# Kernel tuning notes

Hardware: AMD Instinct MI355X
Metric: run time of the kernel (lower is better)

Reference implementation:

```python
import jax, jax.numpy as jnp
import numpy as np


def _pairwise_upper_dists(x):
    # x: [N, D] -> distances for all i<j pairs, shape [N*(N-1)/2]
    n = x.shape[0]
    sq = jnp.sum(x * x, axis=-1)                      # [N]
    d2 = sq[:, None] + sq[None, :] - 2.0 * (x @ x.T)  # [N, N]
    d2 = jnp.maximum(d2, 0.0)
    iu, ju = jnp.triu_indices(n, k=1)                 # matches combinations(range(n), 2)
    return jnp.sqrt(d2[iu, ju])


def setup_inputs() -> dict:
    key = jax.random.key(0)
    k1, k2 = jax.random.split(key)
    pred = jax.random.normal(k1, (1024, 8192), dtype=jnp.float32)
    target = jax.random.normal(k2, (1024, 8192), dtype=jnp.float32)
    return {"pred": pred, "target": target}


def reference(pred, target):
    # all_pairs_in_batch=True branch: Euclidean distance per pair, MSE between
    # the pred-distance vector and the target-distance vector.
    pred_d = _pairwise_upper_dists(pred)      # [P]
    target_d = _pairwise_upper_dists(target)  # [P]
    return jnp.mean((pred_d - target_d) ** 2)
```

## Files before the change

### kernel.cpp

```cpp
#include <hip/hip_runtime.h>
#include <hip/hip_bf16.h>
#include <hip/hip_fp16.h>

#define D 8192
#define NPAIR 523776.0

typedef short short8 __attribute__((ext_vector_type(8)));
typedef float f32x4 __attribute__((ext_vector_type(4)));
typedef _Float16 f16x8 __attribute__((ext_vector_type(8)));

__device__ __forceinline__ short8 cvt8(const float4 a, const float4 b) {
    union { short8 s; __hip_bfloat162 h[4]; } u;
    u.h[0] = __float22bfloat162_rn(make_float2(a.x, a.y));
    u.h[1] = __float22bfloat162_rn(make_float2(a.z, a.w));
    u.h[2] = __float22bfloat162_rn(make_float2(b.x, b.y));
    u.h[3] = __float22bfloat162_rn(make_float2(b.z, b.w));
    return u.s;
}

__device__ __forceinline__ void decode_bid(int bid, int& m, int& ti, int& tj, int& k0, int& nsteps) {
    int x = bid & 7, s = bid >> 3;
    m = x >> 2;
    int xr = x & 3;
    if (s < 16) {
        ti = tj = s & 7;
        int c = ((s >> 3) << 2) + xr;
        k0 = c * 1024; nsteps = 32;
    } else {
        int sp = s - 16;
        int c = (sp / 28) * 4 + xr;
        int tt = sp % 28;
        int a = 0;
        while (tt >= 7 - a) { tt -= 7 - a; ++a; }
        ti = a; tj = a + 1 + tt;
        k0 = c * 512; nsteps = 16;
    }
}
__device__ __forceinline__ int bid_off(int m, int tt, int c) {
    return (m * 4 + (c & 3)) + ((16 + (c >> 2) * 28 + tt) << 3);
}
__device__ __forceinline__ int bid_diag(int m, int dt, int c) {
    return (m * 4 + (c & 3)) + ((((c >> 2) << 3) + dt) << 3);
}

#define GRAM_STEP(S, RA, RB) { \
    const int cur_ = (S) & 1; \
    const short* __restrict__ bufA = lsA[cur_]; \
    const short* __restrict__ bufB = same ? lsA[cur_] : lsB[cur_]; \
    __builtin_amdgcn_s_setprio(1); \
    short8 bf0 = *(const short8*)((const char*)bufB + (rbB + kby)); \
    short8 bf1 = *(const short8*)((const char*)bufB + (rbB + 1024 + kby)); \
    _Pragma("unroll") \
    for (int mi = 0; mi < 4; ++mi) { \
        short8 af = *(const short8*)((const char*)bufA + (rbA + mi * 1024 + kby)); \
        acc[mi][0] = __builtin_amdgcn_mfma_f32_16x16x32_bf16(af, bf0, acc[mi][0], 0, 0, 0); \
        acc[mi][1] = __builtin_amdgcn_mfma_f32_16x16x32_bf16(af, bf1, acc[mi][1], 0, 0, 0); \
    } \
    __builtin_amdgcn_s_setprio(0); \
    if ((S) + 1 < nsteps) { \
        const int nxt_ = cur_ ^ 1; \
        *(short8*)((char*)lsA[nxt_] + wby) = cvt8(RA[0], RA[1]); \
        if (!same) *(short8*)((char*)lsB[nxt_] + wby) = cvt8(RB[0], RB[1]); \
        if ((S) + 3 < nsteps) { \
            const float4* p_ = (const float4*)(gA + ((S) + 3) * 32); \
            RA[0] = p_[0]; RA[1] = p_[1]; \
            if (!same) { \
                const float4* q_ = (const float4*)(gB + ((S) + 3) * 32); \
                RB[0] = q_[0]; RB[1] = q_[1]; \
            } \
        } \
    } \
    asm volatile("s_waitcnt lgkmcnt(0)" ::: "memory"); \
    __builtin_amdgcn_s_barrier(); \
}

template<bool STORE>
__global__ __launch_bounds__(512, 4)
void gram_kernel(const float* __restrict__ pred, const float* __restrict__ tgt,
                 void* __restrict__ outv, float* __restrict__ norms) {
    int m, ti, tj, k0, nsteps;
    decode_bid(blockIdx.x, m, ti, tj, k0, nsteps);
    const bool same = (ti == tj);
    const float* __restrict__ x = m ? tgt : pred;

    __shared__ short lsA[2][4096];
    __shared__ short lsB[2][4096];

    const int tid = threadIdx.x;
    const int lane = tid & 63;
    const int wid = tid >> 6;
    const int wr = wid >> 2, wc = wid & 3;

    const int srow = tid >> 2, sc8 = tid & 3;
    const float* __restrict__ gA = x + (size_t)(ti * 128 + srow) * D + k0 + sc8 * 8;
    const float* __restrict__ gB = x + (size_t)(tj * 128 + srow) * D + k0 + sc8 * 8;
    const int wby = srow * 64 + ((sc8 ^ ((srow >> 1) & 3)) << 4);

    const int rbA = (wr * 64 + (lane & 15)) * 64;
    const int rbB = (wc * 32 + (lane & 15)) * 64;
    const int kby = (((lane >> 4) ^ (((lane & 15) >> 1) & 3)) << 4);

    f32x4 zero = {0.f, 0.f, 0.f, 0.f};
    f32x4 acc[4][2];
#pragma unroll
    for (int mi = 0; mi < 4; ++mi) { acc[mi][0] = zero; acc[mi][1] = zero; }

    float4 raX[2], rbX[2], raY[2], rbY[2];

    { const float4* p = (const float4*)gA; raX[0] = p[0]; raX[1] = p[1];
      if (!same) { const float4* q = (const float4*)gB; rbX[0] = q[0]; rbX[1] = q[1]; } }
    *(short8*)((char*)lsA[0] + wby) = cvt8(raX[0], raX[1]);
    if (!same) *(short8*)((char*)lsB[0] + wby) = cvt8(rbX[0], rbX[1]);
    { const float4* p = (const float4*)(gA + 32); raX[0] = p[0]; raX[1] = p[1];
      if (!same) { const float4* q = (const float4*)(gB + 32); rbX[0] = q[0]; rbX[1] = q[1]; } }
    { const float4* p = (const float4*)(gA + 64); raY[0] = p[0]; raY[1] = p[1];
      if (!same) { const float4* q = (const float4*)(gB + 64); rbY[0] = q[0]; rbY[1] = q[1]; } }
    asm volatile("s_waitcnt lgkmcnt(0)" ::: "memory");
    __builtin_amdgcn_s_barrier();

    for (int sp = 0; sp < nsteps; sp += 2) {
        GRAM_STEP(sp,     raX, rbX)
        GRAM_STEP(sp + 1, raY, rbY)
    }

    if (STORE) {
        __half* __restrict__ dst = (__half*)outv + (size_t)blockIdx.x * 16384;
#pragma unroll
        for (int mi = 0; mi < 4; ++mi)
#pragma unroll
            for (int ni = 0; ni < 2; ++ni)
#pragma unroll
                for (int r = 0; r < 4; ++r) {
                    int li = wr * 64 + mi * 16 + (lane >> 4) * 4 + r;
                    int lj = wc * 32 + ni * 16 + (lane & 15);
                    dst[li * 128 + lj] = __float2half_rn(acc[mi][ni][r]);
                    if (same && li == lj)
                        atomicAdd(&norms[m * 1024 + ti * 128 + li], acc[mi][ni][r]);
                }
    } else {
        float* __restrict__ g = (float*)outv + (size_t)m * (1024 * 1024);
#pragma unroll
        for (int mi = 0; mi < 4; ++mi)
#pragma unroll
            for (int ni = 0; ni < 2; ++ni)
#pragma unroll
                for (int r = 0; r < 4; ++r) {
                    int gi = ti * 128 + wr * 64 + mi * 16 + (lane >> 4) * 4 + r;
                    int gj = tj * 128 + wc * 32 + ni * 16 + (lane & 15);
                    atomicAdd(&g[gi * 1024 + gj], acc[mi][ni][r]);
                }
    }
}

__global__ __launch_bounds__(256)
void loss_store_kernel(const __half* __restrict__ part, const float* __restrict__ norms,
                       float* __restrict__ partial) {
    const int tid = threadIdx.x;
    const int sid = blockIdx.x * 256 + tid;
    const int i  = sid >> 7;
    const int j0 = (sid & 127) << 3;
    float local = 0.f;
    if (j0 + 7 > i) {
        const int ti = i >> 7, tj = j0 >> 7;
        const int el = ((i & 127) << 7) + (j0 & 127);
        float gp[8] = {0,0,0,0,0,0,0,0}, gt[8] = {0,0,0,0,0,0,0,0};
        if (ti == tj) {
#pragma unroll
            for (int c = 0; c < 8; ++c) {
                f16x8 vp = *(const f16x8*)(part + (size_t)bid_diag(0, ti, c) * 16384 + el);
                f16x8 vt = *(const f16x8*)(part + (size_t)bid_diag(1, ti, c) * 16384 + el);
#pragma unroll
                for (int e = 0; e < 8; ++e) { gp[e] += (float)vp[e]; gt[e] += (float)vt[e]; }
            }
        } else {
            int tt = 7 * ti - (ti * (ti - 1)) / 2 + (tj - ti - 1);
#pragma unroll
            for (int c = 0; c < 16; ++c) {
                f16x8 vp = *(const f16x8*)(part + (size_t)bid_off(0, tt, c) * 16384 + el);
                f16x8 vt = *(const f16x8*)(part + (size_t)bid_off(1, tt, c) * 16384 + el);
#pragma unroll
                for (int e = 0; e < 8; ++e) { gp[e] += (float)vp[e]; gt[e] += (float)vt[e]; }
            }
        }
        const float nip = norms[i], nit = norms[1024 + i];
        const float4 njp0 = *(const float4*)(norms + j0);
        const float4 njp1 = *(const float4*)(norms + j0 + 4);
        const float4 njt0 = *(const float4*)(norms + 1024 + j0);
        const float4 njt1 = *(const float4*)(norms + 1024 + j0 + 4);
        const float njp[8] = {njp0.x, njp0.y, njp0.z, njp0.w, njp1.x, njp1.y, njp1.z, njp1.w};
        const float njt[8] = {njt0.x, njt0.y, njt0.z, njt0.w, njt1.x, njt1.y, njt1.z, njt1.w};
#pragma unroll
        for (int e = 0; e < 8; ++e) {
            int j = j0 + e;
            if (j > i) {
                float dp = nip + njp[e] - 2.f * gp[e];
                float dt = nit + njt[e] - 2.f * gt[e];
                float c2 = sqrtf(fmaxf(dp, 0.f)) - sqrtf(fmaxf(dt, 0.f));
                local += c2 * c2;
            }
        }
    }
#pragma unroll
    for (int off = 32; off > 0; off >>= 1) local += __shfl_down(local, off);
    __shared__ float wsum[4];
    if ((tid & 63) == 0) wsum[tid >> 6] = local;
    __syncthreads();
    if (tid == 0) partial[blockIdx.x] = wsum[0] + wsum[1] + wsum[2] + wsum[3];
}

__global__ __launch_bounds__(256)
void loss_atomic_kernel(const float* __restrict__ gram, float* __restrict__ partial) {
    const float* __restrict__ gP = gram;
    const float* __restrict__ gT = gram + 1024 * 1024;
    const int tid = threadIdx.x;
    const int base = blockIdx.x * 256 + tid;
    float local = 0.f;
#pragma unroll
    for (int s = 0; s < 4; ++s) {
        int lin = base + s * 262144;
        int i = lin >> 10, j = lin & 1023;
        if (j > i) {
            float dp = gP[i * 1024 + i] + gP[j * 1024 + j] - 2.f * gP[lin];
            float dt = gT[i * 1024 + i] + gT[j * 1024 + j] - 2.f * gT[lin];
            float c = sqrtf(fmaxf(dp, 0.f)) - sqrtf(fmaxf(dt, 0.f));
            local += c * c;
        }
    }
#pragma unroll
    for (int off = 32; off > 0; off >>= 1) local += __shfl_down(local, off);
    __shared__ float wsum[4];
    if ((tid & 63) == 0) wsum[tid >> 6] = local;
    __syncthreads();
    if (tid == 0) partial[blockIdx.x] = wsum[0] + wsum[1] + wsum[2] + wsum[3];
}

template<int NPART>
__global__ __launch_bounds__(256)
void finalize_kernel(const float* __restrict__ partial, float* __restrict__ out) {
    const int tid = threadIdx.x;
    double local = 0.0;
#pragma unroll
    for (int k = 0; k < NPART / 256; ++k) local += (double)partial[tid + k * 256];
#pragma unroll
    for (int off = 32; off > 0; off >>= 1) local += __shfl_down(local, off);
    __shared__ double wsum[4];
    if ((tid & 63) == 0) wsum[tid >> 6] = local;
    __syncthreads();
    if (tid == 0) out[0] = (float)((wsum[0] + wsum[1] + wsum[2] + wsum[3]) / NPAIR);
}

extern "C" void kernel_launch(void* const* d_in, const int* in_sizes, int n_in,
                              void* d_out, int out_size, void* d_ws, size_t ws_size,
                              hipStream_t stream) {
    const float* pred = (const float*)d_in[0];
    const float* tgt  = (const float*)d_in[1];
    const size_t part_bytes = (size_t)1024 * 16384 * sizeof(__half);
    const size_t need = part_bytes + (2048 + 1024) * sizeof(float);
    if (ws_size >= need) {
        __half* part   = (__half*)d_ws;
        float* norms   = (float*)((char*)d_ws + part_bytes);
        float* partial = norms + 2048;
        hipMemsetAsync(norms, 0, 2048 * sizeof(float), stream);
        gram_kernel<true><<<1024, 512, 0, stream>>>(pred, tgt, (void*)part, norms);
        loss_store_kernel<<<512, 256, 0, stream>>>(part, norms, partial);
        finalize_kernel<512><<<1, 256, 0, stream>>>(partial, (float*)d_out);
    } else {
        float* gram    = (float*)d_ws;
        float* partial = (float*)d_ws + (size_t)2 * 1024 * 1024;
        hipMemsetAsync(gram, 0, (size_t)2 * 1024 * 1024 * sizeof(float), stream);
        gram_kernel<false><<<1024, 512, 0, stream>>>(pred, tgt, (void*)gram, nullptr);
        loss_atomic_kernel<<<1024, 256, 0, stream>>>(gram, partial);
        finalize_kernel<1024><<<1, 256, 0, stream>>>(partial, (float*)d_out);
    }
}
```

Measured before the change: 53.99 us.

## Pre-convert inputs to swizzled bf16 and stream tiles via global_load_lds triple buffer

Adds a separate conversion kernel that writes pred and target as bf16 in a pre-swizzled tile-chunk layout. The Gram kernel then loads those tiles straight into LDS with global_load_lds into a three-deep ring buffer, gated by vmcnt waits, so it no longer spends registers and VALU on fp32 loads and bf16 conversion. This halves the bytes the Gram kernel reads and frees VGPRs, at the cost of an extra pass over the inputs (read fp32, write bf16) and one more launch. The fallback path keeps the old fp32-loading kernel as gram_fb.

Result: slower. 58.17 us (+7.7%).

```diff
diff --git a/kernel.cpp b/kernel.cpp
--- a/kernel.cpp
+++ b/kernel.cpp
@@ -8,6 +8,10 @@
 typedef short short8 __attribute__((ext_vector_type(8)));
 typedef float f32x4 __attribute__((ext_vector_type(4)));
 typedef _Float16 f16x8 __attribute__((ext_vector_type(8)));
+
+#define GLOAD_LDS(G, L) __builtin_amdgcn_global_load_lds( \
+    (const __attribute__((address_space(1))) void*)(G),   \
+    (__attribute__((address_space(3))) void*)(L), 16, 0, 0)
 
 __device__ __forceinline__ short8 cvt8(const float4 a, const float4 b) {
     union { short8 s; __hip_bfloat162 h[4]; } u;
@@ -43,59 +47,69 @@
     return (m * 4 + (c & 3)) + ((((c >> 2) << 3) + dt) << 3);
 }
 
-#define GRAM_STEP(S, RA, RB) { \
-    const int cur_ = (S) & 1; \
-    const short* __restrict__ bufA = lsA[cur_]; \
-    const short* __restrict__ bufB = same ? lsA[cur_] : lsB[cur_]; \
-    __builtin_amdgcn_s_setprio(1); \
-    short8 bf0 = *(const short8*)((const char*)bufB + (rbB + kby)); \
-    short8 bf1 = *(const short8*)((const char*)bufB + (rbB + 1024 + kby)); \
-    _Pragma("unroll") \
-    for (int mi = 0; mi < 4; ++mi) { \
-        short8 af = *(const short8*)((const char*)bufA + (rbA + mi * 1024 + kby)); \
-        acc[mi][0] = __builtin_amdgcn_mfma_f32_16x16x32_bf16(af, bf0, acc[mi][0], 0, 0, 0); \
-        acc[mi][1] = __builtin_amdgcn_mfma_f32_16x16x32_bf16(af, bf1, acc[mi][1], 0, 0, 0); \
+__global__ __launch_bounds__(256)
+void convert_kernel(const float* __restrict__ pred, const float* __restrict__ tgt,
+                    unsigned short* __restrict__ bf) {
+    const int idx = blockIdx.x * 256 + threadIdx.x;
+    const int t = idx & 511;
+    const int c = idx >> 9;
+    const int m = c >> 11, p = (c >> 8) & 7, ks = c & 255;
+    const int rl = t >> 2;
+    const int s = (t & 3) ^ ((rl >> 1) & 3);
+    const float* __restrict__ src = (m ? tgt : pred) + (size_t)(p * 128 + rl) * D + ks * 32 + s * 8;
+    const float4 a = ((const float4*)src)[0];
+    const float4 b = ((const float4*)src)[1];
+    *(short8*)(bf + (size_t)c * 4096 + t * 8) = cvt8(a, b);
+}
+
+#define STAGE(S, COFF) { \
+    GLOAD_LDS(gAc + (size_t)(S) * 8192 + gsub, lsb + (COFF) + wid * 1024); \
+    if (!same) GLOAD_LDS(gBc + (size_t)(S) * 8192 + gsub, lsb + (COFF) + 8192 + wid * 1024); \
+}
+
+#define GSTEP(VMSTR) { \
+    if (sp + 2 < nsteps) STAGE(sp + 2, cN); \
+    { \
+        const char* __restrict__ bA = lsb + cC; \
+        const char* __restrict__ bB = lsb + cC + boff; \
+        __builtin_amdgcn_s_setprio(1); \
+        short8 b0 = *(const short8*)(bB + rbB + kby); \
+        short8 b1 = *(const short8*)(bB + rbB + 1024 + kby); \
+        _Pragma("unroll") \
+        for (int mi = 0; mi < 4; ++mi) { \
+            short8 af = *(const short8*)(bA + rbA + mi * 1024 + kby); \
+            acc[mi][0] = __builtin_amdgcn_mfma_f32_16x16x32_bf16(af, b0, acc[mi][0], 0, 0, 0); \
+            acc[mi][1] = __builtin_amdgcn_mfma_f32_16x16x32_bf16(af, b1, acc[mi][1], 0, 0, 0); \
+        } \
+        __builtin_amdgcn_s_setprio(0); \
     } \
-    __builtin_amdgcn_s_setprio(0); \
-    if ((S) + 1 < nsteps) { \
-        const int nxt_ = cur_ ^ 1; \
-        *(short8*)((char*)lsA[nxt_] + wby) = cvt8(RA[0], RA[1]); \
-        if (!same) *(short8*)((char*)lsB[nxt_] + wby) = cvt8(RB[0], RB[1]); \
-        if ((S) + 3 < nsteps) { \
-            const float4* p_ = (const float4*)(gA + ((S) + 3) * 32); \
-            RA[0] = p_[0]; RA[1] = p_[1]; \
-            if (!same) { \
-                const float4* q_ = (const float4*)(gB + ((S) + 3) * 32); \
-                RB[0] = q_[0]; RB[1] = q_[1]; \
-            } \
-        } \
-    } \
-    asm volatile("s_waitcnt lgkmcnt(0)" ::: "memory"); \
+    if (sp + 2 < nsteps) { asm volatile("s_waitcnt " VMSTR ::: "memory"); } \
+    else                 { asm volatile("s_waitcnt vmcnt(0)" ::: "memory"); } \
     __builtin_amdgcn_s_barrier(); \
-}
-
-template<bool STORE>
+    { int t_ = cC; cC = cM; cM = cN; cN = t_; } \
+    ++sp; \
+}
+
 __global__ __launch_bounds__(512, 4)
-void gram_kernel(const float* __restrict__ pred, const float* __restrict__ tgt,
-                 void* __restrict__ outv, float* __restrict__ norms) {
+void gram_kernel(const unsigned short* __restrict__ bf, __half* __restrict__ part,
+                 float* __restrict__ norms) {
     int m, ti, tj, k0, nsteps;
     decode_bid(blockIdx.x, m, ti, tj, k0, nsteps);
     const bool same = (ti == tj);
-    const float* __restrict__ x = m ? tgt : pred;
-
-    __shared__ short lsA[2][4096];
-    __shared__ short lsB[2][4096];
+
+    __shared__ short ls[24576];
+    char* lsb = (char*)ls;
 
     const int tid = threadIdx.x;
     const int lane = tid & 63;
     const int wid = tid >> 6;
     const int wr = wid >> 2, wc = wid & 3;
 
-    const int srow = tid >> 2, sc8 = tid & 3;
-    const float* __restrict__ gA = x + (size_t)(ti * 128 + srow) * D + k0 + sc8 * 8;
-    const float* __restrict__ gB = x + (size_t)(tj * 128 + srow) * D + k0 + sc8 * 8;
-    const int wby = srow * 64 + ((sc8 ^ ((srow >> 1) & 3)) << 4);
-
+    const char* __restrict__ gAc = (const char*)(bf + (size_t)(m * 2048 + ti * 256 + (k0 >> 5)) * 4096);
+    const char* __restrict__ gBc = (const char*)(bf + (size_t)(m * 2048 + tj * 256 + (k0 >> 5)) * 4096);
+    const int gsub = wid * 1024 + lane * 16;
+
+    const int boff = same ? 0 : 8192;
     const int rbA = (wr * 64 + (lane & 15)) * 64;
     const int rbB = (wc * 32 + (lane & 15)) * 64;
     const int kby = (((lane >> 4) ^ (((lane & 15) >> 1) & 3)) << 4);
@@ -105,51 +119,31 @@
 #pragma unroll
     for (int mi = 0; mi < 4; ++mi) { acc[mi][0] = zero; acc[mi][1] = zero; }
 
-    float4 raX[2], rbX[2], raY[2], rbY[2];
-
-    { const float4* p = (const float4*)gA; raX[0] = p[0]; raX[1] = p[1];
-      if (!same) { const float4* q = (const float4*)gB; rbX[0] = q[0]; rbX[1] = q[1]; } }
-    *(short8*)((char*)lsA[0] + wby) = cvt8(raX[0], raX[1]);
-    if (!same) *(short8*)((char*)lsB[0] + wby) = cvt8(rbX[0], rbX[1]);
-    { const float4* p = (const float4*)(gA + 32); raX[0] = p[0]; raX[1] = p[1];
-      if (!same) { const float4* q = (const float4*)(gB + 32); rbX[0] = q[0]; rbX[1] = q[1]; } }
-    { const float4* p = (const float4*)(gA + 64); raY[0] = p[0]; raY[1] = p[1];
-      if (!same) { const float4* q = (const float4*)(gB + 64); rbY[0] = q[0]; rbY[1] = q[1]; } }
-    asm volatile("s_waitcnt lgkmcnt(0)" ::: "memory");
+    int cC = 0, cM = 16384, cN = 32768;
+
+    STAGE(0, cC)
+    STAGE(1, cM)
+    if (same) { asm volatile("s_waitcnt vmcnt(1)" ::: "memory"); }
+    else      { asm volatile("s_waitcnt vmcnt(2)" ::: "memory"); }
     __builtin_amdgcn_s_barrier();
 
-    for (int sp = 0; sp < nsteps; sp += 2) {
-        GRAM_STEP(sp,     raX, rbX)
-        GRAM_STEP(sp + 1, raY, rbY)
-    }
-
-    if (STORE) {
-        __half* __restrict__ dst = (__half*)outv + (size_t)blockIdx.x * 16384;
-#pragma unroll
-        for (int mi = 0; mi < 4; ++mi)
-#pragma unroll
-            for (int ni = 0; ni < 2; ++ni)
-#pragma unroll
-                for (int r = 0; r < 4; ++r) {
-                    int li = wr * 64 + mi * 16 + (lane >> 4) * 4 + r;
-                    int lj = wc * 32 + ni * 16 + (lane & 15);
-                    dst[li * 128 + lj] = __float2half_rn(acc[mi][ni][r]);
-                    if (same && li == lj)
-                        atomicAdd(&norms[m * 1024 + ti * 128 + li], acc[mi][ni][r]);
-                }
-    } else {
-        float* __restrict__ g = (float*)outv + (size_t)m * (1024 * 1024);
-#pragma unroll
-        for (int mi = 0; mi < 4; ++mi)
-#pragma unroll
-            for (int ni = 0; ni < 2; ++ni)
-#pragma unroll
-                for (int r = 0; r < 4; ++r) {
-                    int gi = ti * 128 + wr * 64 + mi * 16 + (lane >> 4) * 4 + r;
-                    int gj = tj * 128 + wc * 32 + ni * 16 + (lane & 15);
-                    atomicAdd(&g[gi * 1024 + gj], acc[mi][ni][r]);
-                }
-    }
+    int sp = 0;
+    if (same) { while (sp < nsteps) { GSTEP("vmcnt(1)") } }
+    else      { while (sp < nsteps) { GSTEP("vmcnt(2)") } }
+
+    __half* __restrict__ dst = part + (size_t)blockIdx.x * 16384;
+#pragma unroll
+    for (int mi = 0; mi < 4; ++mi)
+#pragma unroll
+        for (int ni = 0; ni < 2; ++ni)
+#pragma unroll
+            for (int r = 0; r < 4; ++r) {
+                int li = wr * 64 + mi * 16 + (lane >> 4) * 4 + r;
+                int lj = wc * 32 + ni * 16 + (lane & 15);
+                dst[li * 128 + lj] = __float2half_rn(acc[mi][ni][r]);
+                if (same && li == lj)
+                    atomicAdd(&norms[m * 1024 + ti * 128 + li], acc[mi][ni][r]);
+            }
 }
 
 __global__ __launch_bounds__(256)
@@ -208,6 +202,91 @@
     if (tid == 0) partial[blockIdx.x] = wsum[0] + wsum[1] + wsum[2] + wsum[3];
 }
 
+template<int NPART>
+__global__ __launch_bounds__(256)
+void finalize_kernel(const float* __restrict__ partial, float* __restrict__ out) {
+    const int tid = threadIdx.x;
+    double local = 0.0;
+#pragma unroll
+    for (int k = 0; k < NPART / 256; ++k) local += (double)partial[tid + k * 256];
+#pragma unroll
+    for (int off = 32; off > 0; off >>= 1) local += __shfl_down(local, off);
+    __shared__ double wsum[4];
+    if ((tid & 63) == 0) wsum[tid >> 6] = local;
+    __syncthreads();
+    if (tid == 0) out[0] = (float)((wsum[0] + wsum[1] + wsum[2] + wsum[3]) / NPAIR);
+}
+
+__global__ __launch_bounds__(512)
+void gram_fb(const float* __restrict__ pred, const float* __restrict__ tgt,
+             float* __restrict__ g4) {
+    int m, ti, tj, k0, nsteps;
+    decode_bid(blockIdx.x, m, ti, tj, k0, nsteps);
+    const bool same = (ti == tj);
+    const float* __restrict__ x = m ? tgt : pred;
+    __shared__ short lsA[2][4096];
+    __shared__ short lsB[2][4096];
+    const int tid = threadIdx.x;
+    const int lane = tid & 63;
+    const int wid = tid >> 6;
+    const int wr = wid >> 2, wc = wid & 3;
+    const int srow = tid >> 2, sc8 = tid & 3;
+    const float* __restrict__ gA = x + (size_t)(ti * 128 + srow) * D + k0 + sc8 * 8;
+    const float* __restrict__ gB = x + (size_t)(tj * 128 + srow) * D + k0 + sc8 * 8;
+    const int wby = srow * 64 + ((sc8 ^ ((srow >> 1) & 3)) << 4);
+    const int rbA = (wr * 64 + (lane & 15)) * 64;
+    const int rbB = (wc * 32 + (lane & 15)) * 64;
+    const int kby = (((lane >> 4) ^ (((lane & 15) >> 1) & 3)) << 4);
+    f32x4 zero = {0.f, 0.f, 0.f, 0.f};
+    f32x4 acc[4][2];
+#pragma unroll
+    for (int mi = 0; mi < 4; ++mi) { acc[mi][0] = zero; acc[mi][1] = zero; }
+    float4 ra0, ra1, rb0, rb1;
+    { const float4* p = (const float4*)gA; ra0 = p[0]; ra1 = p[1];
+      if (!same) { const float4* q = (const float4*)gB; rb0 = q[0]; rb1 = q[1]; } }
+    *(short8*)((char*)lsA[0] + wby) = cvt8(ra0, ra1);
+    if (!same) *(short8*)((char*)lsB[0] + wby) = cvt8(rb0, rb1);
+    { const float4* p = (const float4*)(gA + 32); ra0 = p[0]; ra1 = p[1];
+      if (!same) { const float4* q = (const float4*)(gB + 32); rb0 = q[0]; rb1 = q[1]; } }
+    asm volatile("s_waitcnt lgkmcnt(0)" ::: "memory");
+    __builtin_amdgcn_s_barrier();
+    for (int step = 0; step < nsteps; ++step) {
+        const int cur = step & 1;
+        const short* __restrict__ bufA = lsA[cur];
+        const short* __restrict__ bufB = same ? lsA[cur] : lsB[cur];
+        short8 bf0 = *(const short8*)((const char*)bufB + (rbB + kby));
+        short8 bf1 = *(const short8*)((const char*)bufB + (rbB + 1024 + kby));
+#pragma unroll
+        for (int mi = 0; mi < 4; ++mi) {
+            short8 af = *(const short8*)((const char*)bufA + (rbA + mi * 1024 + kby));
+            acc[mi][0] = __builtin_amdgcn_mfma_f32_16x16x32_bf16(af, bf0, acc[mi][0], 0, 0, 0);
+            acc[mi][1] = __builtin_amdgcn_mfma_f32_16x16x32_bf16(af, bf1, acc[mi][1], 0, 0, 0);
+        }
+        if (step + 1 < nsteps) {
+            const int nxt = cur ^ 1;
+            *(short8*)((char*)lsA[nxt] + wby) = cvt8(ra0, ra1);
+            if (!same) *(short8*)((char*)lsB[nxt] + wby) = cvt8(rb0, rb1);
+            if (step + 2 < nsteps) {
+                const float4* p = (const float4*)(gA + (step + 2) * 32);
+                ra0 = p[0]; ra1 = p[1];
+                if (!same) { const float4* q = (const float4*)(gB + (step + 2) * 32); rb0 = q[0]; rb1 = q[1]; }
+            }
+        }
+        asm volatile("s_waitcnt lgkmcnt(0)" ::: "memory");
+        __builtin_amdgcn_s_barrier();
+    }
+#pragma unroll
+    for (int mi = 0; mi < 4; ++mi)
+#pragma unroll
+        for (int ni = 0; ni < 2; ++ni)
+#pragma unroll
+            for (int r = 0; r < 4; ++r) {
+                int gi = ti * 128 + wr * 64 + mi * 16 + (lane >> 4) * 4 + r;
+                int gj = tj * 128 + wc * 32 + ni * 16 + (lane & 15);
+                atomicAdd(&g4[(size_t)m * 1048576 + gi * 1024 + gj], acc[mi][ni][r]);
+            }
+}
+
 __global__ __launch_bounds__(256)
 void loss_atomic_kernel(const float* __restrict__ gram, float* __restrict__ partial) {
     const float* __restrict__ gP = gram;
@@ -234,41 +313,29 @@
     if (tid == 0) partial[blockIdx.x] = wsum[0] + wsum[1] + wsum[2] + wsum[3];
 }
 
-template<int NPART>
-__global__ __launch_bounds__(256)
-void finalize_kernel(const float* __restrict__ partial, float* __restrict__ out) {
-    const int tid = threadIdx.x;
-    double local = 0.0;
-#pragma unroll
-    for (int k = 0; k < NPART / 256; ++k) local += (double)partial[tid + k * 256];
-#pragma unroll
-    for (int off = 32; off > 0; off >>= 1) local += __shfl_down(local, off);
-    __shared__ double wsum[4];
-    if ((tid & 63) == 0) wsum[tid >> 6] = local;
-    __syncthreads();
-    if (tid == 0) out[0] = (float)((wsum[0] + wsum[1] + wsum[2] + wsum[3]) / NPAIR);
-}
-
 extern "C" void kernel_launch(void* const* d_in, const int* in_sizes, int n_in,
                               void* d_out, int out_size, void* d_ws, size_t ws_size,
                               hipStream_t stream) {
     const float* pred = (const float*)d_in[0];
     const float* tgt  = (const float*)d_in[1];
-    const size_t part_bytes = (size_t)1024 * 16384 * sizeof(__half);
-    const size_t need = part_bytes + (2048 + 1024) * sizeof(float);
+    const size_t bf_bytes   = (size_t)4096 * 4096 * 2;
+    const size_t part_bytes = (size_t)1024 * 16384 * 2;
+    const size_t need = bf_bytes + part_bytes + (2048 + 512) * sizeof(float);
     if (ws_size >= need) {
-        __half* part   = (__half*)d_ws;
-        float* norms   = (float*)((char*)d_ws + part_bytes);
+        unsigned short* bfbuf = (unsigned short*)d_ws;
+        __half* part   = (__half*)((char*)d_ws + bf_bytes);
+        float* norms   = (float*)((char*)part + part_bytes);
         float* partial = norms + 2048;
         hipMemsetAsync(norms, 0, 2048 * sizeof(float), stream);
-        gram_kernel<true><<<1024, 512, 0, stream>>>(pred, tgt, (void*)part, norms);
+        convert_kernel<<<8192, 256, 0, stream>>>(pred, tgt, bfbuf);
+        gram_kernel<<<1024, 512, 0, stream>>>(bfbuf, part, norms);
         loss_store_kernel<<<512, 256, 0, stream>>>(part, norms, partial);
         finalize_kernel<512><<<1, 256, 0, stream>>>(partial, (float*)d_out);
     } else {
         float* gram    = (float*)d_ws;
         float* partial = (float*)d_ws + (size_t)2 * 1024 * 1024;
         hipMemsetAsync(gram, 0, (size_t)2 * 1024 * 1024 * sizeof(float), stream);
-        gram_kernel<false><<<1024, 512, 0, stream>>>(pred, tgt, (void*)gram, nullptr);
+        gram_fb<<<1024, 512, 0, stream>>>(pred, tgt, gram);
         loss_atomic_kernel<<<1024, 256, 0, stream>>>(gram, partial);
         finalize_kernel<1024><<<1, 256, 0, stream>>>(partial, (float*)d_out);
     }
```
